# Kernel tuning notes

Measured on AMD Instinct MI355X. Metric: run time of the kernel, lower is better.

The kernel has to match this reference:

```python
import jax, jax.numpy as jnp
import numpy as np

N_NODES = 100000
N_EDGES = 1600000
IN_DIM = 64
HIDDEN_DIM = 64


def setup_inputs() -> dict:
    key = jax.random.key(0)
    ks = jax.random.split(key, 8)
    x = jax.random.normal(ks[0], (N_NODES, IN_DIM), dtype=jnp.float32)
    edge_index = jax.random.randint(ks[1], (2, N_EDGES), 0, N_NODES, dtype=jnp.int32)
    s = 1.0 / np.sqrt(IN_DIM)
    sh = 1.0 / np.sqrt(HIDDEN_DIM)
    # SAGEConv params: lin_l (applied to mean-aggregated neighbors, with bias),
    # lin_r (applied to root/self features, no bias) -- PyG defaults.
    w1l = jax.random.uniform(ks[2], (IN_DIM, HIDDEN_DIM), jnp.float32, -s, s)
    b1l = jax.random.uniform(ks[3], (HIDDEN_DIM,), jnp.float32, -s, s)
    w1r = jax.random.uniform(ks[4], (IN_DIM, HIDDEN_DIM), jnp.float32, -s, s)
    w2l = jax.random.uniform(ks[5], (HIDDEN_DIM, HIDDEN_DIM), jnp.float32, -sh, sh)
    b2l = jax.random.uniform(ks[6], (HIDDEN_DIM,), jnp.float32, -sh, sh)
    w2r = jax.random.uniform(ks[7], (HIDDEN_DIM, HIDDEN_DIM), jnp.float32, -sh, sh)
    return {"x": x, "edge_index": edge_index, "w1l": w1l, "b1l": b1l,
            "w1r": w1r, "w2l": w2l, "b2l": b2l, "w2r": w2r}


def reference(x, edge_index, w1l, b1l, w1r, w2l, b2l, w2r):
    n = x.shape[0]
    src, dst = edge_index[0], edge_index[1]
    # in-degree (number of incoming messages per target node), clamped to 1
    deg = jax.ops.segment_sum(jnp.ones(src.shape, x.dtype), dst, num_segments=n)
    inv_deg = 1.0 / jnp.maximum(deg, 1.0)  # [N]

    def sage_conv(h, wl, bl, wr):
        # mean aggregation of neighbor messages: scatter-add then normalize
        agg = jax.ops.segment_sum(h[src], dst, num_segments=n) * inv_deg[:, None]
        return agg @ wl + bl + h @ wr

    h = jax.nn.relu(sage_conv(x, w1l, b1l, w1r))  # conv1 + relu
    return sage_conv(h, w2l, b2l, w2r)            # conv2 (no activation)
```

## Files before the change

kernel.cpp:

```cpp
#include <hip/hip_runtime.h>
#include <hip/hip_fp16.h>


#define DIM 64
#define BN 64
#define MAXBUCK 2048
#define CHUNK 8192
#define GCAP 2048
#define WT_STRIDE 72

using f16x8 = __attribute__((ext_vector_type(8))) _Float16;
using f32x4 = __attribute__((ext_vector_type(4))) float;

__device__ inline void addh8(float* acc, float4 raw) {
    const __half2* hp = (const __half2*)&raw;
#pragma unroll
    for (int k = 0; k < 4; ++k) {
        float2 f = __half22float2(hp[k]);
        acc[2 * k]     += f.x;
        acc[2 * k + 1] += f.y;
    }
}

__global__ __launch_bounds__(256) void prehist_kernel(const int* __restrict__ dst,
                                                      int* __restrict__ ghist,
                                                      int nE, int nbuck) {
    __shared__ int hist[MAXBUCK];
    const int t = threadIdx.x;
    for (int k = t; k < nbuck; k += 256) hist[k] = 0;
    __syncthreads();
    const int base = blockIdx.x * CHUNK;
    const int end = min(nE, base + CHUNK);
    for (int i = base + t; i < end; i += 256)
        atomicAdd(&hist[dst[i] >> 6], 1);
    __syncthreads();
    for (int k = t; k < nbuck; k += 256)
        if (hist[k]) atomicAdd(&ghist[k], hist[k]);
}

__global__ __launch_bounds__(1024) void scan_kernel(const int* __restrict__ ghist,
                                                    int* __restrict__ boff,
                                                    int* __restrict__ gcur, int nbuck) {
    __shared__ int sa[2048], sb[2048];
    const int t = threadIdx.x;
    int v0 = (t < nbuck) ? ghist[t] : 0;
    int v1 = (t + 1024 < nbuck) ? ghist[t + 1024] : 0;
    sa[t] = v0; sa[t + 1024] = v1;
    __syncthreads();
    int* in = sa; int* out = sb;
    for (int d = 1; d < 2048; d <<= 1) {
        out[t] = in[t] + ((t >= d) ? in[t - d] : 0);
        int i2 = t + 1024;
        out[i2] = in[i2] + ((i2 >= d) ? in[i2 - d] : 0);
        __syncthreads();
        int* tmp = in; in = out; out = tmp;
    }
    if (t < nbuck) { int e = in[t] - v0; boff[t] = e; gcur[t] = e; }
    if (t + 1024 < nbuck) { int e = in[t + 1024] - v1; boff[t + 1024] = e; gcur[t + 1024] = e; }
    if (t == 0) boff[nbuck] = in[2047];
}

__device__ inline void load_bfrag(const float* __restrict__ H, long long nn, int lq,
                                  f16x8& b0, f16x8& b1) {
    const float* p = &H[nn * 64 + lq * 8];
    float4 u0 = *(const float4*)p;
    float4 u1 = *(const float4*)(p + 4);
    float4 u2 = *(const float4*)(p + 32);
    float4 u3 = *(const float4*)(p + 36);
    b0[0] = (_Float16)u0.x; b0[1] = (_Float16)u0.y; b0[2] = (_Float16)u0.z; b0[3] = (_Float16)u0.w;
    b0[4] = (_Float16)u1.x; b0[5] = (_Float16)u1.y; b0[6] = (_Float16)u1.z; b0[7] = (_Float16)u1.w;
    b1[0] = (_Float16)u2.x; b1[1] = (_Float16)u2.y; b1[2] = (_Float16)u2.z; b1[3] = (_Float16)u2.w;
    b1[4] = (_Float16)u3.x; b1[5] = (_Float16)u3.y; b1[6] = (_Float16)u3.z; b1[7] = (_Float16)u3.w;
}

__device__ void gemm_body(int bid, __half* wt,
                          const float* __restrict__ H,
                          const float* __restrict__ Wl, const float* __restrict__ Wr,
                          const float* __restrict__ bias,
                          __half* __restrict__ A, __half* __restrict__ Dbuf, int n) {
    const int t = threadIdx.x;
    for (int i = t; i < 4096; i += 256) {
        int k = i >> 6, m = i & 63;
        wt[(size_t)m * WT_STRIDE + k] = __float2half(Wl[i]);
        wt[(size_t)(64 + m) * WT_STRIDE + k] = __float2half(Wr[i]);
    }
    __syncthreads();
    const int lane = t & 63, wave = t >> 6;
    const int ln = lane & 15, lq = lane >> 4;
    f16x8 af[2][4][2];
#pragma unroll
    for (int mat = 0; mat < 2; ++mat)
#pragma unroll
        for (int mt = 0; mt < 4; ++mt)
#pragma unroll
            for (int ki = 0; ki < 2; ++ki)
                af[mat][mt][ki] = *(const f16x8*)&wt[(size_t)(mat * 64 + mt * 16 + ln) * WT_STRIDE
                                                     + ki * 32 + lq * 8];
    float4 bf[4];
#pragma unroll
    for (int mt = 0; mt < 4; ++mt)
        bf[mt] = *(const float4*)&bias[mt * 16 + lq * 4];

    const int base = bid * 256;
    for (int it = 0; it < 4; ++it) {
        const int node = base + it * 64 + wave * 16 + ln;
        const long long nn = (node < n) ? node : (n - 1);
        f16x8 b0, b1;
        load_bfrag(H, nn, lq, b0, b1);
        f32x4 acc[2][4];
#pragma unroll
        for (int mat = 0; mat < 2; ++mat)
#pragma unroll
            for (int mt = 0; mt < 4; ++mt) {
                f32x4 z = {0.f, 0.f, 0.f, 0.f};
                z = __builtin_amdgcn_mfma_f32_16x16x32_f16(af[mat][mt][0], b0, z, 0, 0, 0);
                z = __builtin_amdgcn_mfma_f32_16x16x32_f16(af[mat][mt][1], b1, z, 0, 0, 0);
                acc[mat][mt] = z;
            }
        if (node < n) {
#pragma unroll
            for (int mt = 0; mt < 4; ++mt) {
                union { __half2 h[2]; float2 f; } u;
                u.h[0] = __floats2half2_rn(acc[0][mt][0], acc[0][mt][1]);
                u.h[1] = __floats2half2_rn(acc[0][mt][2], acc[0][mt][3]);
                *(float2*)&A[(size_t)node * 64 + mt * 16 + lq * 4] = u.f;
                union { __half2 h[2]; float2 f; } v;
                v.h[0] = __floats2half2_rn(acc[1][mt][0] + bf[mt].x, acc[1][mt][1] + bf[mt].y);
                v.h[1] = __floats2half2_rn(acc[1][mt][2] + bf[mt].z, acc[1][mt][3] + bf[mt].w);
                *(float2*)&Dbuf[(size_t)node * 64 + mt * 16 + lq * 4] = v.f;
            }
        }
    }
}

__global__ __launch_bounds__(256) void part_gemm_kernel(const int* __restrict__ src,
                                                        const int* __restrict__ dst,
                                                        int* __restrict__ gcur,
                                                        unsigned* __restrict__ P,
                                                        int nE, int nbuck, int pb,
                                                        const float* __restrict__ H,
                                                        const float* __restrict__ Wl,
                                                        const float* __restrict__ Wr,
                                                        const float* __restrict__ bias,
                                                        __half* __restrict__ A,
                                                        __half* __restrict__ Dbuf, int n) {
    __shared__ __align__(16) unsigned short smem_u[2 * 64 * WT_STRIDE];
    if ((int)blockIdx.x < pb) {
        int* hist = (int*)smem_u;
        const int t = threadIdx.x;
        for (int k = t; k < nbuck; k += 256) hist[k] = 0;
        __syncthreads();
        const int base = blockIdx.x * CHUNK;
        const int end = min(nE, base + CHUNK);
        for (int i = base + t; i < end; i += 256)
            atomicAdd(&hist[dst[i] >> 6], 1);
        __syncthreads();
        for (int k = t; k < nbuck; k += 256) {
            int h = hist[k];
            hist[k] = h ? atomicAdd(&gcur[k], h) : 0;
        }
        __syncthreads();
        for (int i = base + t; i < end; i += 256) {
            int d = dst[i];
            int bk = d >> 6;
            int pos = atomicAdd(&hist[bk], 1);
            P[pos] = ((unsigned)src[i] << 6) | (unsigned)(d & 63);
        }
    } else {
        gemm_body(blockIdx.x - pb, (__half*)smem_u, H, Wl, Wr, bias, A, Dbuf, n);
    }
}

__global__ __launch_bounds__(256) void gather_gemm_kernel(const __half* __restrict__ A,
                                                          const __half* Din,
                                                          const int* __restrict__ boff,
                                                          const unsigned* __restrict__ P,
                                                          int* __restrict__ spill,
                                                          const float* __restrict__ Wl,
                                                          const float* __restrict__ Wr,
                                                          const float* __restrict__ bias,
                                                          __half* __restrict__ A2,
                                                          __half* D2, int n) {
    __shared__ int hist[BN];
    __shared__ int rstart[BN];
    __shared__ int cur[BN];
    __shared__ int lsrc[GCAP];
    __shared__ __align__(16) __half wt[2 * 64 * WT_STRIDE];
    __shared__ __align__(16) __half tile[64 * WT_STRIDE];
    const int t = threadIdx.x;
    const int b = blockIdx.x;
    for (int i = t; i < 4096; i += 256) {
        int k = i >> 6, m = i & 63;
        wt[(size_t)m * WT_STRIDE + k] = __float2half(Wl[i]);
        wt[(size_t)(64 + m) * WT_STRIDE + k] = __float2half(Wr[i]);
    }
    if (t < BN) hist[t] = 0;
    __syncthreads();
    const int start = boff[b], end = boff[b + 1];
    const int nedge = end - start;
    for (int i = start + t; i < end; i += 256)
        atomicAdd(&hist[P[i] & 63], 1);
    __syncthreads();
    if (t < 64) {
        int v = hist[t];
        int s = v;
#pragma unroll
        for (int d = 1; d < 64; d <<= 1) {
            int u = __shfl_up(s, d);
            if (t >= d) s += u;
        }
        rstart[t] = s - v;
        cur[t] = s - v;
    }
    __syncthreads();
    int* list = (nedge <= GCAP) ? (int*)lsrc : (spill + start);
    for (int i = start + t; i < end; i += 256) {
        unsigned p = P[i];
        int pos = atomicAdd(&cur[p & 63], 1);
        list[pos] = (int)(p >> 6);
    }
    __syncthreads();
    const int dg = t & 7;
    const size_t doff = (size_t)dg * 8;
    for (int pass = 0; pass < 2; ++pass) {
        const int r = pass * 32 + (t >> 3);
        const int node = b * BN + r;
        float o[8] = {0.f, 0.f, 0.f, 0.f, 0.f, 0.f, 0.f, 0.f};
        if (node < n) {
            const int c = hist[r];
            const int* sp = list + rstart[r];
            float acc[8] = {0.f, 0.f, 0.f, 0.f, 0.f, 0.f, 0.f, 0.f};
            int j = 0;
            for (; j + 4 <= c; j += 4) {
                int e0 = sp[j + 0], e1 = sp[j + 1], e2 = sp[j + 2], e3 = sp[j + 3];
                float4 r0 = *(const float4*)&A[(size_t)e0 * 64 + doff];
                float4 r1 = *(const float4*)&A[(size_t)e1 * 64 + doff];
                float4 r2 = *(const float4*)&A[(size_t)e2 * 64 + doff];
                float4 r3 = *(const float4*)&A[(size_t)e3 * 64 + doff];
                addh8(acc, r0); addh8(acc, r1); addh8(acc, r2); addh8(acc, r3);
            }
            for (; j < c; ++j) {
                float4 rr = *(const float4*)&A[(size_t)sp[j] * 64 + doff];
                addh8(acc, rr);
            }
            const float inv = 1.0f / fmaxf((float)c, 1.0f);
            float d8[8] = {0.f, 0.f, 0.f, 0.f, 0.f, 0.f, 0.f, 0.f};
            addh8(d8, *(const float4*)&Din[(size_t)node * 64 + doff]);
#pragma unroll
            for (int k = 0; k < 8; ++k)
                o[k] = fmaxf(fmaf(acc[k], inv, d8[k]), 0.f);
        }
        union { __half2 h[4]; float4 f; } u;
#pragma unroll
        for (int k = 0; k < 4; ++k)
            u.h[k] = __floats2half2_rn(o[2 * k], o[2 * k + 1]);
        *(float4*)&tile[(size_t)r * WT_STRIDE + doff] = u.f;
    }
    __syncthreads();
    const int lane = t & 63, wave = t >> 6;
    const int ln = lane & 15, lq = lane >> 4;
    f16x8 af[2][4][2];
#pragma unroll
    for (int mat = 0; mat < 2; ++mat)
#pragma unroll
        for (int mt = 0; mt < 4; ++mt)
#pragma unroll
            for (int ki = 0; ki < 2; ++ki)
                af[mat][mt][ki] = *(const f16x8*)&wt[(size_t)(mat * 64 + mt * 16 + ln) * WT_STRIDE
                                                     + ki * 32 + lq * 8];
    float4 bf[4];
#pragma unroll
    for (int mt = 0; mt < 4; ++mt)
        bf[mt] = *(const float4*)&bias[mt * 16 + lq * 4];

    const int r = wave * 16 + ln;
    f16x8 b0 = *(const f16x8*)&tile[(size_t)r * WT_STRIDE + lq * 8];
    f16x8 b1 = *(const f16x8*)&tile[(size_t)r * WT_STRIDE + 32 + lq * 8];
    f32x4 acc2[2][4];
#pragma unroll
    for (int mat = 0; mat < 2; ++mat)
#pragma unroll
        for (int mt = 0; mt < 4; ++mt) {
            f32x4 z = {0.f, 0.f, 0.f, 0.f};
            z = __builtin_amdgcn_mfma_f32_16x16x32_f16(af[mat][mt][0], b0, z, 0, 0, 0);
            z = __builtin_amdgcn_mfma_f32_16x16x32_f16(af[mat][mt][1], b1, z, 0, 0, 0);
            acc2[mat][mt] = z;
        }
    const int node = b * BN + r;
    if (node < n) {
#pragma unroll
        for (int mt = 0; mt < 4; ++mt) {
            union { __half2 h[2]; float2 f; } u;
            u.h[0] = __floats2half2_rn(acc2[0][mt][0], acc2[0][mt][1]);
            u.h[1] = __floats2half2_rn(acc2[0][mt][2], acc2[0][mt][3]);
            *(float2*)&A2[(size_t)node * 64 + mt * 16 + lq * 4] = u.f;
            union { __half2 h[2]; float2 f; } v;
            v.h[0] = __floats2half2_rn(acc2[1][mt][0] + bf[mt].x, acc2[1][mt][1] + bf[mt].y);
            v.h[1] = __floats2half2_rn(acc2[1][mt][2] + bf[mt].z, acc2[1][mt][3] + bf[mt].w);
            *(float2*)&D2[(size_t)node * 64 + mt * 16 + lq * 4] = v.f;
        }
    }
}

template <bool RELU, typename OutT>
__global__ __launch_bounds__(256) void gather_sort_combine(const __half* __restrict__ A,
                                                           const __half* __restrict__ Dbuf,
                                                           const int* __restrict__ boff,
                                                           const unsigned* __restrict__ P,
                                                           int* __restrict__ spill,
                                                           OutT* __restrict__ out, int n) {
    __shared__ int hist[BN];
    __shared__ int rstart[BN];
    __shared__ int cur[BN];
    __shared__ int lsrc[GCAP];
    const int t = threadIdx.x;
    const int b = blockIdx.x;
    if (t < BN) hist[t] = 0;
    __syncthreads();
    const int start = boff[b], end = boff[b + 1];
    const int m = end - start;
    for (int i = start + t; i < end; i += 256)
        atomicAdd(&hist[P[i] & 63], 1);
    __syncthreads();
    if (t < 64) {
        int v = hist[t];
        int s = v;
#pragma unroll
        for (int d = 1; d < 64; d <<= 1) {
            int u = __shfl_up(s, d);
            if (t >= d) s += u;
        }
        rstart[t] = s - v;
        cur[t] = s - v;
    }
    __syncthreads();
    int* list = (m <= GCAP) ? (int*)lsrc : (spill + start);
    for (int i = start + t; i < end; i += 256) {
        unsigned p = P[i];
        int pos = atomicAdd(&cur[p & 63], 1);
        list[pos] = (int)(p >> 6);
    }
    __syncthreads();
    const int dg = t & 7;
    const size_t doff = (size_t)dg * 8;
    for (int pass = 0; pass < 2; ++pass) {
        const int r = pass * 32 + (t >> 3);
        const int node = b * BN + r;
        if (node >= n) continue;
        const int c = hist[r];
        const int* sp = list + rstart[r];
        float acc[8] = {0.f, 0.f, 0.f, 0.f, 0.f, 0.f, 0.f, 0.f};
        int j = 0;
        for (; j + 4 <= c; j += 4) {
            int e0 = sp[j + 0], e1 = sp[j + 1], e2 = sp[j + 2], e3 = sp[j + 3];
            float4 r0 = *(const float4*)&A[(size_t)e0 * 64 + doff];
            float4 r1 = *(const float4*)&A[(size_t)e1 * 64 + doff];
            float4 r2 = *(const float4*)&A[(size_t)e2 * 64 + doff];
            float4 r3 = *(const float4*)&A[(size_t)e3 * 64 + doff];
            addh8(acc, r0); addh8(acc, r1); addh8(acc, r2); addh8(acc, r3);
        }
        for (; j < c; ++j) {
            float4 rr = *(const float4*)&A[(size_t)sp[j] * 64 + doff];
            addh8(acc, rr);
        }
        const float inv = 1.0f / fmaxf((float)c, 1.0f);
        float d8[8] = {0, 0, 0, 0, 0, 0, 0, 0};
        addh8(d8, *(const float4*)&Dbuf[(size_t)node * 64 + doff]);
        float o[8];
#pragma unroll
        for (int k = 0; k < 8; ++k) {
            float v = fmaf(acc[k], inv, d8[k]);
            o[k] = RELU ? fmaxf(v, 0.f) : v;
        }
        if constexpr (sizeof(OutT) == 2) {
            union { __half2 h[4]; float4 f; } u;
#pragma unroll
            for (int k = 0; k < 4; ++k)
                u.h[k] = __floats2half2_rn(o[2 * k], o[2 * k + 1]);
            *(float4*)&out[(size_t)node * 64 + doff] = u.f;
        } else {
            *(float4*)&out[(size_t)node * 64 + doff]     = make_float4(o[0], o[1], o[2], o[3]);
            *(float4*)&out[(size_t)node * 64 + doff + 4] = make_float4(o[4], o[5], o[6], o[7]);
        }
    }
}

extern "C" void kernel_launch(void* const* d_in, const int* in_sizes, int n_in,
                              void* d_out, int out_size, void* d_ws, size_t ws_size,
                              hipStream_t stream) {
    const float* x   = (const float*)d_in[0];
    const int*   ei  = (const int*)d_in[1];
    const float* w1l = (const float*)d_in[2];
    const float* b1l = (const float*)d_in[3];
    const float* w1r = (const float*)d_in[4];
    const float* w2l = (const float*)d_in[5];
    const float* b2l = (const float*)d_in[6];
    const float* w2r = (const float*)d_in[7];
    float* out = (float*)d_out;

    const int N = in_sizes[0] / DIM;
    const int E = in_sizes[1] / 2;
    const int* src = ei;
    const int* dst = ei + E;
    const int nbuck = (N + BN - 1) / BN;
    const int pb = (E + CHUNK - 1) / CHUNK;
    const int gb = (N + 255) / 256;

    int* ghist = (int*)d_ws;
    int* boff = ghist + nbuck;
    int* gcur = boff + nbuck + 1;
    unsigned* P = (unsigned*)(gcur + nbuck);
    int* spill = (int*)(P + E);
    uintptr_t ap = (uintptr_t)(spill + E);
    ap = (ap + 15) & ~(uintptr_t)15;
    __half* A  = (__half*)ap;
    __half* D  = A + (size_t)N * DIM;
    __half* A2 = D + (size_t)N * DIM;

    hipMemsetAsync(ghist, 0, nbuck * sizeof(int), stream);
    prehist_kernel<<<pb, 256, 0, stream>>>(dst, ghist, E, nbuck);
    scan_kernel<<<1, 1024, 0, stream>>>(ghist, boff, gcur, nbuck);
    part_gemm_kernel<<<pb + gb, 256, 0, stream>>>(src, dst, gcur, P, E, nbuck, pb,
                                                  x, w1l, w1r, b1l, A, D, N);

    gather_gemm_kernel<<<nbuck, 256, 0, stream>>>(A, D, boff, P, spill,
                                                  w2l, w2r, b2l, A2, D, N);

    gather_sort_combine<false, float><<<nbuck, 256, 0, stream>>>(A2, D, boff, P, spill, out, N);
}
```

Measured before the change: 270.6 us.

## Materialize per-node CSR in first gather and reuse it in final combine

The first gather kernel now writes the locally sorted source list to a global P2 array and per-node start offsets, building a full CSR. The final combine kernel reads that CSR directly instead of redoing the per-bucket histogram, scan and scatter sort. The shared-memory staging list is dropped, so the first gather always writes through global memory, which may raise its traffic. The partition chunk size is also halved.

```diff
diff --git a/kernel.cpp b/kernel.cpp
--- a/kernel.cpp
+++ b/kernel.cpp
@@ -5,8 +5,7 @@
 #define DIM 64
 #define BN 64
 #define MAXBUCK 2048
-#define CHUNK 8192
-#define GCAP 2048
+#define CHUNK 4096
 #define WT_STRIDE 72
 
 using f16x8 = __attribute__((ext_vector_type(8))) _Float16;
@@ -175,7 +174,8 @@
                                                           const __half* Din,
                                                           const int* __restrict__ boff,
                                                           const unsigned* __restrict__ P,
-                                                          int* __restrict__ spill,
+                                                          int* __restrict__ P2,
+                                                          int* __restrict__ nstart,
                                                           const float* __restrict__ Wl,
                                                           const float* __restrict__ Wr,
                                                           const float* __restrict__ bias,
@@ -184,7 +184,6 @@
     __shared__ int hist[BN];
     __shared__ int rstart[BN];
     __shared__ int cur[BN];
-    __shared__ int lsrc[GCAP];
     __shared__ __align__(16) __half wt[2 * 64 * WT_STRIDE];
     __shared__ __align__(16) __half tile[64 * WT_STRIDE];
     const int t = threadIdx.x;
@@ -197,7 +196,6 @@
     if (t < BN) hist[t] = 0;
     __syncthreads();
     const int start = boff[b], end = boff[b + 1];
-    const int nedge = end - start;
     for (int i = start + t; i < end; i += 256)
         atomicAdd(&hist[P[i] & 63], 1);
     __syncthreads();
@@ -213,11 +211,15 @@
         cur[t] = s - v;
     }
     __syncthreads();
-    int* list = (nedge <= GCAP) ? (int*)lsrc : (spill + start);
+    if (t < 64) {
+        int node = b * BN + t;
+        if (node < n) nstart[node] = start + rstart[t];
+    }
+    if (b == 0 && t == 0) nstart[n] = boff[gridDim.x];
     for (int i = start + t; i < end; i += 256) {
         unsigned p = P[i];
         int pos = atomicAdd(&cur[p & 63], 1);
-        list[pos] = (int)(p >> 6);
+        P2[start + pos] = (int)(p >> 6);
     }
     __syncthreads();
     const int dg = t & 7;
@@ -228,7 +230,7 @@
         float o[8] = {0.f, 0.f, 0.f, 0.f, 0.f, 0.f, 0.f, 0.f};
         if (node < n) {
             const int c = hist[r];
-            const int* sp = list + rstart[r];
+            const int* sp = P2 + start + rstart[r];
             float acc[8] = {0.f, 0.f, 0.f, 0.f, 0.f, 0.f, 0.f, 0.f};
             int j = 0;
             for (; j + 4 <= c; j += 4) {
@@ -302,53 +304,22 @@
     }
 }
 
-template <bool RELU, typename OutT>
-__global__ __launch_bounds__(256) void gather_sort_combine(const __half* __restrict__ A,
-                                                           const __half* __restrict__ Dbuf,
-                                                           const int* __restrict__ boff,
-                                                           const unsigned* __restrict__ P,
-                                                           int* __restrict__ spill,
-                                                           OutT* __restrict__ out, int n) {
-    __shared__ int hist[BN];
-    __shared__ int rstart[BN];
-    __shared__ int cur[BN];
-    __shared__ int lsrc[GCAP];
+__global__ __launch_bounds__(256) void gather_csr_combine(const __half* __restrict__ A,
+                                                          const __half* __restrict__ Dbuf,
+                                                          const int* __restrict__ nstart,
+                                                          const int* __restrict__ P2,
+                                                          float* __restrict__ out, int n) {
     const int t = threadIdx.x;
     const int b = blockIdx.x;
-    if (t < BN) hist[t] = 0;
-    __syncthreads();
-    const int start = boff[b], end = boff[b + 1];
-    const int m = end - start;
-    for (int i = start + t; i < end; i += 256)
-        atomicAdd(&hist[P[i] & 63], 1);
-    __syncthreads();
-    if (t < 64) {
-        int v = hist[t];
-        int s = v;
-#pragma unroll
-        for (int d = 1; d < 64; d <<= 1) {
-            int u = __shfl_up(s, d);
-            if (t >= d) s += u;
-        }
-        rstart[t] = s - v;
-        cur[t] = s - v;
-    }
-    __syncthreads();
-    int* list = (m <= GCAP) ? (int*)lsrc : (spill + start);
-    for (int i = start + t; i < end; i += 256) {
-        unsigned p = P[i];
-        int pos = atomicAdd(&cur[p & 63], 1);
-        list[pos] = (int)(p >> 6);
-    }
-    __syncthreads();
     const int dg = t & 7;
     const size_t doff = (size_t)dg * 8;
     for (int pass = 0; pass < 2; ++pass) {
         const int r = pass * 32 + (t >> 3);
         const int node = b * BN + r;
         if (node >= n) continue;
-        const int c = hist[r];
-        const int* sp = list + rstart[r];
+        const int s0 = nstart[node];
+        const int c = nstart[node + 1] - s0;
+        const int* sp = P2 + s0;
         float acc[8] = {0.f, 0.f, 0.f, 0.f, 0.f, 0.f, 0.f, 0.f};
         int j = 0;
         for (; j + 4 <= c; j += 4) {
@@ -364,24 +335,14 @@
             addh8(acc, rr);
         }
         const float inv = 1.0f / fmaxf((float)c, 1.0f);
-        float d8[8] = {0, 0, 0, 0, 0, 0, 0, 0};
+        float d8[8] = {0.f, 0.f, 0.f, 0.f, 0.f, 0.f, 0.f, 0.f};
         addh8(d8, *(const float4*)&Dbuf[(size_t)node * 64 + doff]);
         float o[8];
 #pragma unroll
-        for (int k = 0; k < 8; ++k) {
-            float v = fmaf(acc[k], inv, d8[k]);
-            o[k] = RELU ? fmaxf(v, 0.f) : v;
-        }
-        if constexpr (sizeof(OutT) == 2) {
-            union { __half2 h[4]; float4 f; } u;
-#pragma unroll
-            for (int k = 0; k < 4; ++k)
-                u.h[k] = __floats2half2_rn(o[2 * k], o[2 * k + 1]);
-            *(float4*)&out[(size_t)node * 64 + doff] = u.f;
-        } else {
-            *(float4*)&out[(size_t)node * 64 + doff]     = make_float4(o[0], o[1], o[2], o[3]);
-            *(float4*)&out[(size_t)node * 64 + doff + 4] = make_float4(o[4], o[5], o[6], o[7]);
-        }
+        for (int k = 0; k < 8; ++k)
+            o[k] = fmaf(acc[k], inv, d8[k]);
+        *(float4*)&out[(size_t)node * 64 + doff]     = make_float4(o[0], o[1], o[2], o[3]);
+        *(float4*)&out[(size_t)node * 64 + doff + 4] = make_float4(o[4], o[5], o[6], o[7]);
     }
 }
 
@@ -410,8 +371,9 @@
     int* boff = ghist + nbuck;
     int* gcur = boff + nbuck + 1;
     unsigned* P = (unsigned*)(gcur + nbuck);
-    int* spill = (int*)(P + E);
-    uintptr_t ap = (uintptr_t)(spill + E);
+    int* P2 = (int*)(P + E);
+    int* nstart = P2 + E;
+    uintptr_t ap = (uintptr_t)(nstart + N + 1);
     ap = (ap + 15) & ~(uintptr_t)15;
     __half* A  = (__half*)ap;
     __half* D  = A + (size_t)N * DIM;
@@ -423,8 +385,8 @@
     part_gemm_kernel<<<pb + gb, 256, 0, stream>>>(src, dst, gcur, P, E, nbuck, pb,
                                                   x, w1l, w1r, b1l, A, D, N);
 
-    gather_gemm_kernel<<<nbuck, 256, 0, stream>>>(A, D, boff, P, spill,
+    gather_gemm_kernel<<<nbuck, 256, 0, stream>>>(A, D, boff, P, P2, nstart,
                                                   w2l, w2r, b2l, A2, D, N);
 
-    gather_sort_combine<false, float><<<nbuck, 256, 0, stream>>>(A2, D, boff, P, spill, out, N);
-}
+    gather_csr_combine<<<nbuck, 256, 0, stream>>>(A2, D, nstart, P2, out, N);
+}
```

Result: slower. 279.4 us (+3.2%).
